# Performance work log

Hardware: AMD Instinct MI355X
Metric: run time of the kernel (lower is better)

Reference implementation:

```python
import jax, jax.numpy as jnp
import numpy as np

N_TASKS = 32
SCALING = 32.0 / 16.0  # lora_alpha / r


def setup_inputs() -> dict:
    key = jax.random.key(0)
    k = jax.random.split(key, 6)
    B_, D_IN, D_OUT, R = 32768, 1024, 1024, 16
    x = jax.random.normal(k[0], (B_, D_IN), dtype=jnp.float32)
    task_ids = jax.random.randint(k[1], (B_,), 0, N_TASKS, dtype=jnp.int32)
    W_base = jax.random.normal(k[2], (D_OUT, D_IN), dtype=jnp.float32) * 0.02
    b_base = jax.random.normal(k[3], (D_OUT,), dtype=jnp.float32) * 0.02
    A = jax.random.normal(k[4], (N_TASKS, R, D_IN), dtype=jnp.float32) * 0.02
    B = jax.random.normal(k[5], (N_TASKS, D_OUT, R), dtype=jnp.float32) * 0.02
    return {"x": x, "task_ids": task_ids, "W_base": W_base, "b_base": b_base, "A": A, "B": B}


def reference(x, task_ids, W_base, b_base, A, B):
    # Base linear: [B, D_in] @ [D_in, D_out] + bias
    result = x @ W_base.T + b_base
    # Per-example task routing. Equivalent to gathering A[t], B[t] per row,
    # expressed as a masked dense contraction over the small task axis.
    onehot = jax.nn.one_hot(task_ids, N_TASKS, dtype=x.dtype)  # [B, T]
    # down-projection for every task, then mask to the selected task: [B, T, r]
    ax = jnp.einsum('bi,tri->btr', x, A) * onehot[:, :, None]
    # up-projection contracting out the task axis: [B, D_out]
    lora_out = jnp.einsum('btr,tor->bo', ax, B) * SCALING
    return result + lora_out
```

## Files before the change

kernel.cpp:

```cpp
#include <hip/hip_runtime.h>


#define D_IN   1024
#define D_OUTV 1024
#define NTASK  32
#define NROWS  32768
#define RLORA  16
#define SCALE  2.0f

typedef unsigned short u16;
typedef __attribute__((ext_vector_type(4))) unsigned short u16x4;
typedef __attribute__((ext_vector_type(8))) unsigned short u16x8;
typedef __attribute__((ext_vector_type(8))) short s16x8;
typedef __attribute__((ext_vector_type(4))) float f32x4;

#define WB_OFF   (0)
#define AB_OFF   (2*1024*1024)
#define BB_OFF   (3*1024*1024)
#define CNT_OFF  (4*1024*1024)
#define RIDX_OFF (CNT_OFF + 512)
#define XG_OFF   (8ull*1024*1024)

__device__ __forceinline__ u16 f2bf(float f) {
  union { float f; unsigned u; } v; v.f = f;
  unsigned r = v.u + 0x7fffu + ((v.u >> 16) & 1u);
  return (u16)(r >> 16);
}

__device__ __forceinline__ void gl2lds16(const void* g, void* s) {
  __builtin_amdgcn_global_load_lds(
      (const __attribute__((address_space(1))) unsigned*)g,
      (__attribute__((address_space(3))) unsigned*)s, 16, 0, 0);
}

__global__ void k_convert(const float* __restrict__ W, const float* __restrict__ A,
                          const float* __restrict__ B, u16* __restrict__ Wb,
                          u16* __restrict__ Ab, u16* __restrict__ Bb) {
  int g = blockIdx.x * blockDim.x + threadIdx.x;
  const int NW = D_OUTV * D_IN / 4;
  const int NA = NTASK * RLORA * D_IN / 4;
  const float* src; u16* dst; int idx;
  if (g < NW) { src = W; dst = Wb; idx = g; }
  else if (g < NW + NA) { src = A; dst = Ab; idx = g - NW; }
  else { src = B; dst = Bb; idx = g - NW - NA; }
  f32x4 v = *(const f32x4*)(src + (size_t)idx * 4);
  u16x4 o;
  o[0] = f2bf(v[0]); o[1] = f2bf(v[1]); o[2] = f2bf(v[2]); o[3] = f2bf(v[3]);
  *(u16x4*)(dst + (size_t)idx * 4) = o;
}

__global__ void k_hist(const int* __restrict__ tasks, int* __restrict__ cnt) {
  __shared__ int h[NTASK];
  int tid = threadIdx.x;
  if (tid < NTASK) h[tid] = 0;
  __syncthreads();
  atomicAdd(&h[tasks[blockIdx.x * 256 + tid]], 1);
  __syncthreads();
  if (tid < NTASK) atomicAdd(&cnt[tid], h[tid]);
}

__global__ void k_scan(int* __restrict__ cnt) {
  int t = threadIdx.x;
  int c = (t < NTASK) ? cnt[t] : 0;
  int v = c;
  for (int d = 1; d < NTASK; d <<= 1) {
    int u = __shfl_up(v, d, 64);
    if (t >= d) v += u;
  }
  if (t < NTASK) {
    int ex = v - c;
    cnt[64 + t] = ex;
    cnt[32 + t] = ex;
    if (t == NTASK - 1) cnt[64 + NTASK] = v;
  }
}

__global__ void k_scatter(const int* __restrict__ tasks, int* __restrict__ cnt,
                          int* __restrict__ ridx) {
  __shared__ int h[NTASK], basev[NTASK];
  int tid = threadIdx.x;
  int b = blockIdx.x * 256 + tid;
  int t = tasks[b];
  if (tid < NTASK) h[tid] = 0;
  __syncthreads();
  atomicAdd(&h[t], 1);
  __syncthreads();
  if (tid < NTASK) {
    basev[tid] = atomicAdd(&cnt[32 + tid], h[tid]);
    h[tid] = 0;
  }
  __syncthreads();
  int r = atomicAdd(&h[t], 1);
  ridx[basev[t] + r] = b;
}

__global__ void k_gatherx(const float* __restrict__ x, const int* __restrict__ ridx,
                          u16* __restrict__ xg) {
  int g = blockIdx.x * 256 + threadIdx.x;
  int pos = g >> 7;
  int c8  = (g & 127) << 3;
  int src = ridx[pos];
  f32x4 a = *(const f32x4*)(x + (size_t)src * D_IN + c8);
  f32x4 b = *(const f32x4*)(x + (size_t)src * D_IN + c8 + 4);
  u16x8 o;
  o[0] = f2bf(a[0]); o[1] = f2bf(a[1]); o[2] = f2bf(a[2]); o[3] = f2bf(a[3]);
  o[4] = f2bf(b[0]); o[5] = f2bf(b[1]); o[6] = f2bf(b[2]); o[7] = f2bf(b[3]);
  *(u16x8*)(xg + (size_t)pos * D_IN + c8) = o;
}

#define BM 256
#define BN 128
#define BK 64
#define NTHR 512
#define SLOTS 5
#define NWG (8 * NTASK * SLOTS)

#define XSZ (BM * BK)
#define WSZ (BN * BK)
#define ASZ (RLORA * BK)

__global__ __launch_bounds__(NTHR, 2) void k_main_c(
    const u16* __restrict__ xg, const float* __restrict__ bias,
    const u16* __restrict__ Wb, const u16* __restrict__ Ab, const u16* __restrict__ Bb,
    const int* __restrict__ cnt, const int* __restrict__ ridx,
    float* __restrict__ out) {
  __shared__ __align__(16) u16 smem[2 * XSZ + 2 * WSZ + 2 * ASZ];
  __shared__ u16 bls[BN * 32];
  __shared__ u16 axs[BM * 32];
  __shared__ int rowid_l[BM];
  u16* xs  = smem;
  u16* wls = smem + 2 * XSZ;
  u16* als = wls + 2 * WSZ;
  float* ostage = (float*)smem;

  const int tid = threadIdx.x;
  const int l   = tid & 63;
  const int w   = tid >> 6;
  const int wr  = w >> 1;
  const int wc  = w & 1;
  const int l15 = l & 15;
  const int lg  = l >> 4;

  const int flat = blockIdx.x;
  const int idx  = flat >> 3;
  const int task = (flat & 7) + ((idx & 3) << 3);
  const int rem  = idx >> 2;
  const int cb   = rem & 7;
  const int slot = rem >> 3;

  const int o0    = cnt[64 + task];
  const int count = cnt[64 + task + 1] - o0;
  const int base  = slot * BM;
  if (base >= count) return;

  auto stage = [&](int t, int bsel) {
    const int kk = t * BK;
    u16* xbuf = xs + bsel * XSZ;
    u16* wbuf = wls + bsel * WSZ;
    u16* abuf = als + bsel * ASZ;
#pragma unroll
    for (int i = 0; i < 4; i++) {
      int ch = i * NTHR + tid;
      int r = ch >> 3, c = ch & 7;
      int gr = o0 + base + r;
      if (gr > NROWS - 1) gr = NROWS - 1;
      gl2lds16(xg + (size_t)gr * D_IN + kk + ((c ^ (r & 7)) << 3), xbuf + ch * 8);
    }
#pragma unroll
    for (int i = 0; i < 2; i++) {
      int ch = i * NTHR + tid;
      int wrow = ch >> 3, c = ch & 7;
      gl2lds16(Wb + (size_t)(cb * BN + wrow) * D_IN + kk + ((c ^ (wrow & 7)) << 3),
               wbuf + ch * 8);
    }
    if (tid < 128) {
      int r = tid >> 3, c = tid & 7;
      gl2lds16(Ab + (size_t)(task * RLORA + r) * D_IN + kk + ((c ^ (r & 7)) << 3),
               abuf + tid * 8);
    }
  };

  f32x4 acc[4][4];
  f32x4 axc[4];
  const f32x4 z4 = {0.f, 0.f, 0.f, 0.f};
#pragma unroll
  for (int m = 0; m < 4; m++) {
    axc[m] = z4;
#pragma unroll
    for (int n = 0; n < 4; n++) acc[m][n] = z4;
  }

  stage(0, 0);
  for (int s = tid; s < BN * 4; s += NTHR) {
    int c = s >> 2, part = s & 3;
    u16x8 v = {0, 0, 0, 0, 0, 0, 0, 0};
    if (part < 2)
      v = *(const u16x8*)(Bb + ((size_t)(task * D_OUTV) + cb * BN + c) * RLORA + part * 8);
    *(u16x8*)&bls[c * 32 + ((part * 8) ^ ((c & 3) << 3))] = v;
  }
  for (int i = tid; i < BM * 32 / 8; i += NTHR) {
    u16x8 z = {0, 0, 0, 0, 0, 0, 0, 0};
    *(u16x8*)&axs[i * 8] = z;
  }
  if (tid < BM) {
    int s = base + tid;
    rowid_l[tid] = (s < count) ? ridx[o0 + s] : 0;
  }
  __syncthreads();

#pragma unroll 2
  for (int t = 0; t < D_IN / BK; ++t) {
    if (t < D_IN / BK - 1) stage(t + 1, (t + 1) & 1);
    const u16* xbuf = xs + (t & 1) * XSZ;
    const u16* wbuf = wls + (t & 1) * WSZ;
    const u16* abuf = als + (t & 1) * ASZ;
#pragma unroll
    for (int k0 = 0; k0 < BK; k0 += 32) {
      int kf = k0 + lg * 8;
      s16x8 xf[4], wf[4];
#pragma unroll
      for (int m = 0; m < 4; m++) {
        int row = wr * 64 + m * 16 + l15;
        xf[m] = *(const s16x8*)&xbuf[row * BK + (kf ^ ((row & 7) << 3))];
      }
#pragma unroll
      for (int n = 0; n < 4; n++) {
        int col = wc * 64 + n * 16 + l15;
        wf[n] = *(const s16x8*)&wbuf[col * BK + (kf ^ ((col & 7) << 3))];
      }
#pragma unroll
      for (int m = 0; m < 4; m++)
#pragma unroll
        for (int n = 0; n < 4; n++)
          acc[m][n] = __builtin_amdgcn_mfma_f32_16x16x32_bf16(xf[m], wf[n], acc[m][n], 0, 0, 0);
      if (wc == 0) {
        s16x8 af = *(const s16x8*)&abuf[l15 * BK + (kf ^ ((l15 & 7) << 3))];
#pragma unroll
        for (int m = 0; m < 4; m++)
          axc[m] = __builtin_amdgcn_mfma_f32_16x16x32_bf16(xf[m], af, axc[m], 0, 0, 0);
      }
    }
    __syncthreads();
  }

  if (wc == 0) {
#pragma unroll
    for (int m = 0; m < 4; m++) {
#pragma unroll
      for (int j = 0; j < 4; j++) {
        int row = wr * 64 + m * 16 + lg * 4 + j;
        axs[row * 32 + (l15 ^ ((row & 3) << 3))] = f2bf(axc[m][j] * SCALE);
      }
    }
  }
  __syncthreads();

  int kf2 = lg * 8;
  s16x8 axf[4], blf[4];
#pragma unroll
  for (int m = 0; m < 4; m++) {
    int row = wr * 64 + m * 16 + l15;
    axf[m] = *(const s16x8*)&axs[row * 32 + (kf2 ^ ((row & 3) << 3))];
  }
#pragma unroll
  for (int n = 0; n < 4; n++) {
    int col = wc * 64 + n * 16 + l15;
    blf[n] = *(const s16x8*)&bls[col * 32 + (kf2 ^ ((col & 3) << 3))];
  }
  float bv[4];
#pragma unroll
  for (int n = 0; n < 4; n++) bv[n] = bias[cb * BN + wc * 64 + n * 16 + l15];
#pragma unroll
  for (int n = 0; n < 4; n++)
#pragma unroll
    for (int m = 0; m < 4; m++) {
      acc[m][n] = __builtin_amdgcn_mfma_f32_16x16x32_bf16(axf[m], blf[n], acc[m][n], 0, 0, 0);
#pragma unroll
      for (int j = 0; j < 4; j++) acc[m][n][j] += bv[n];
    }

#pragma unroll
  for (int half = 0; half < 2; ++half) {
    __syncthreads();
    if ((wr >> 1) == half) {
#pragma unroll
      for (int m = 0; m < 4; m++)
#pragma unroll
        for (int n = 0; n < 4; n++)
#pragma unroll
          for (int j = 0; j < 4; j++) {
            int rl  = (wr & 1) * 64 + m * 16 + lg * 4 + j;
            int col = wc * 64 + n * 16 + l15;
            ostage[rl * 128 + (col ^ (((rl >> 2) & 3) << 3))] = acc[m][n][j];
          }
    }
    __syncthreads();
#pragma unroll
    for (int it = 0; it < 8; ++it) {
      int ch = it * NTHR + tid;
      int rl = ch >> 5;
      int cq = ch & 31;
      int lrow = half * 128 + rl;
      if (base + lrow < count) {
        int grow = rowid_l[lrow];
        f32x4 v = *(const f32x4*)&ostage[rl * 128 + ((cq * 4) ^ (((rl >> 2) & 3) << 3))];
        *(f32x4*)&out[(size_t)grow * D_OUTV + cb * BN + cq * 4] = v;
      }
    }
  }
}

extern "C" void kernel_launch(void* const* d_in, const int* in_sizes, int n_in,
                              void* d_out, int out_size, void* d_ws, size_t ws_size,
                              hipStream_t stream) {
  const float* x     = (const float*)d_in[0];
  const int*   tasks = (const int*)d_in[1];
  const float* W     = (const float*)d_in[2];
  const float* bias  = (const float*)d_in[3];
  const float* A     = (const float*)d_in[4];
  const float* B     = (const float*)d_in[5];
  float* out = (float*)d_out;
  char* ws = (char*)d_ws;
  u16* Wb = (u16*)(ws + WB_OFF);
  u16* Ab = (u16*)(ws + AB_OFF);
  u16* Bb = (u16*)(ws + BB_OFF);
  int* cnt  = (int*)(ws + CNT_OFF);
  int* ridx = (int*)(ws + RIDX_OFF);
  u16* xg   = (u16*)(ws + XG_OFF);

  hipMemsetAsync(cnt, 0, 512, stream);
  k_convert<<<2048, 256, 0, stream>>>(W, A, B, Wb, Ab, Bb);
  k_hist<<<NROWS / 256, 256, 0, stream>>>(tasks, cnt);
  k_scan<<<1, 64, 0, stream>>>(cnt);
  k_scatter<<<NROWS / 256, 256, 0, stream>>>(tasks, cnt, ridx);
  k_gatherx<<<NROWS * D_IN / 8 / 256, 256, 0, stream>>>(x, ridx, xg);
  k_main_c<<<NWG, NTHR, 0, stream>>>(xg, bias, Wb, Ab, Bb, cnt, ridx, out);
}
```

Baseline: 183.0 us.

## Preload LoRA A slice fully, use explicit vmcnt waits, write outputs directly

Loads the task's full 16x1024 LoRA A block into LDS once at the start instead of staging a 64-column slice per k-step. The per-iteration __syncthreads is replaced by raw s_barrier plus an explicit s_waitcnt vmcnt(6), which lets the next stage's global-to-LDS loads stay in flight while the current tile is computed. The LDS-staged coalesced float4 epilogue is dropped in favour of scattered scalar stores from MFMA registers. That removes two barriers and the staging traffic, but the stores become less coalesced and LDS use grows, which may hurt occupancy at two blocks per CU.

```diff
diff --git a/kernel.cpp b/kernel.cpp
--- a/kernel.cpp
+++ b/kernel.cpp
@@ -115,23 +115,22 @@
 #define SLOTS 5
 #define NWG (8 * NTASK * SLOTS)
 
-#define XSZ (BM * BK)
-#define WSZ (BN * BK)
-#define ASZ (RLORA * BK)
+#define XSZ  (BM * BK)
+#define WSZ  (BN * BK)
+#define ALSZ (RLORA * D_IN)
+#define NKS  (D_IN / BK)
 
 __global__ __launch_bounds__(NTHR, 2) void k_main_c(
     const u16* __restrict__ xg, const float* __restrict__ bias,
     const u16* __restrict__ Wb, const u16* __restrict__ Ab, const u16* __restrict__ Bb,
     const int* __restrict__ cnt, const int* __restrict__ ridx,
     float* __restrict__ out) {
-  __shared__ __align__(16) u16 smem[2 * XSZ + 2 * WSZ + 2 * ASZ];
+  __shared__ __align__(16) u16 xs[2 * XSZ];
+  __shared__ __align__(16) u16 wls[2 * WSZ];
+  __shared__ __align__(16) u16 als[ALSZ];
   __shared__ u16 bls[BN * 32];
   __shared__ u16 axs[BM * 32];
   __shared__ int rowid_l[BM];
-  u16* xs  = smem;
-  u16* wls = smem + 2 * XSZ;
-  u16* als = wls + 2 * WSZ;
-  float* ostage = (float*)smem;
 
   const int tid = threadIdx.x;
   const int l   = tid & 63;
@@ -157,7 +156,6 @@
     const int kk = t * BK;
     u16* xbuf = xs + bsel * XSZ;
     u16* wbuf = wls + bsel * WSZ;
-    u16* abuf = als + bsel * ASZ;
 #pragma unroll
     for (int i = 0; i < 4; i++) {
       int ch = i * NTHR + tid;
@@ -173,24 +171,8 @@
       gl2lds16(Wb + (size_t)(cb * BN + wrow) * D_IN + kk + ((c ^ (wrow & 7)) << 3),
                wbuf + ch * 8);
     }
-    if (tid < 128) {
-      int r = tid >> 3, c = tid & 7;
-      gl2lds16(Ab + (size_t)(task * RLORA + r) * D_IN + kk + ((c ^ (r & 7)) << 3),
-               abuf + tid * 8);
-    }
   };
 
-  f32x4 acc[4][4];
-  f32x4 axc[4];
-  const f32x4 z4 = {0.f, 0.f, 0.f, 0.f};
-#pragma unroll
-  for (int m = 0; m < 4; m++) {
-    axc[m] = z4;
-#pragma unroll
-    for (int n = 0; n < 4; n++) acc[m][n] = z4;
-  }
-
-  stage(0, 0);
   for (int s = tid; s < BN * 4; s += NTHR) {
     int c = s >> 2, part = s & 3;
     u16x8 v = {0, 0, 0, 0, 0, 0, 0, 0};
@@ -208,12 +190,41 @@
   }
   __syncthreads();
 
+#pragma unroll
+  for (int i = 0; i < 4; i++) {
+    int ch = i * NTHR + tid;
+    int r = ch >> 7, c = ch & 127;
+    gl2lds16(Ab + (size_t)(task * RLORA + r) * D_IN + ((c ^ (r & 7)) << 3),
+             als + ch * 8);
+  }
+  stage(0, 0);
+
+  f32x4 acc[4][4];
+  f32x4 axc[4];
+  const f32x4 z4 = {0.f, 0.f, 0.f, 0.f};
+#pragma unroll
+  for (int m = 0; m < 4; m++) {
+    axc[m] = z4;
+#pragma unroll
+    for (int n = 0; n < 4; n++) acc[m][n] = z4;
+  }
+
 #pragma unroll 2
-  for (int t = 0; t < D_IN / BK; ++t) {
-    if (t < D_IN / BK - 1) stage(t + 1, (t + 1) & 1);
+  for (int t = 0; t < NKS; ++t) {
+    asm volatile("" ::: "memory");
+    __builtin_amdgcn_s_barrier();
+    asm volatile("" ::: "memory");
+    if (t < NKS - 1) stage(t + 1, (t + 1) & 1);
+    if (t < NKS - 1) {
+      asm volatile("s_waitcnt vmcnt(6)" ::: "memory");
+    } else {
+      asm volatile("s_waitcnt vmcnt(0)" ::: "memory");
+    }
+    __builtin_amdgcn_s_barrier();
+    __builtin_amdgcn_sched_barrier(0);
+
     const u16* xbuf = xs + (t & 1) * XSZ;
     const u16* wbuf = wls + (t & 1) * WSZ;
-    const u16* abuf = als + (t & 1) * ASZ;
 #pragma unroll
     for (int k0 = 0; k0 < BK; k0 += 32) {
       int kf = k0 + lg * 8;
@@ -234,14 +245,15 @@
         for (int n = 0; n < 4; n++)
           acc[m][n] = __builtin_amdgcn_mfma_f32_16x16x32_bf16(xf[m], wf[n], acc[m][n], 0, 0, 0);
       if (wc == 0) {
-        s16x8 af = *(const s16x8*)&abuf[l15 * BK + (kf ^ ((l15 & 7) << 3))];
+        int kg = t * BK + kf;
+        s16x8 af = *(const s16x8*)&als[l15 * D_IN + (kg ^ ((l15 & 7) << 3))];
 #pragma unroll
         for (int m = 0; m < 4; m++)
           axc[m] = __builtin_amdgcn_mfma_f32_16x16x32_bf16(xf[m], af, axc[m], 0, 0, 0);
       }
     }
-    __syncthreads();
-  }
+  }
+  __syncthreads();
 
   if (wc == 0) {
 #pragma unroll
@@ -271,40 +283,18 @@
 #pragma unroll
   for (int n = 0; n < 4; n++) bv[n] = bias[cb * BN + wc * 64 + n * 16 + l15];
 #pragma unroll
-  for (int n = 0; n < 4; n++)
+  for (int n = 0; n < 4; n++) {
+    int colg = cb * BN + wc * 64 + n * 16 + l15;
 #pragma unroll
     for (int m = 0; m < 4; m++) {
-      acc[m][n] = __builtin_amdgcn_mfma_f32_16x16x32_bf16(axf[m], blf[n], acc[m][n], 0, 0, 0);
-#pragma unroll
-      for (int j = 0; j < 4; j++) acc[m][n][j] += bv[n];
-    }
-
-#pragma unroll
-  for (int half = 0; half < 2; ++half) {
-    __syncthreads();
-    if ((wr >> 1) == half) {
-#pragma unroll
-      for (int m = 0; m < 4; m++)
-#pragma unroll
-        for (int n = 0; n < 4; n++)
-#pragma unroll
-          for (int j = 0; j < 4; j++) {
-            int rl  = (wr & 1) * 64 + m * 16 + lg * 4 + j;
-            int col = wc * 64 + n * 16 + l15;
-            ostage[rl * 128 + (col ^ (((rl >> 2) & 3) << 3))] = acc[m][n][j];
-          }
-    }
-    __syncthreads();
-#pragma unroll
-    for (int it = 0; it < 8; ++it) {
-      int ch = it * NTHR + tid;
-      int rl = ch >> 5;
-      int cq = ch & 31;
-      int lrow = half * 128 + rl;
-      if (base + lrow < count) {
-        int grow = rowid_l[lrow];
-        f32x4 v = *(const f32x4*)&ostage[rl * 128 + ((cq * 4) ^ (((rl >> 2) & 3) << 3))];
-        *(f32x4*)&out[(size_t)grow * D_OUTV + cb * BN + cq * 4] = v;
+      f32x4 r = __builtin_amdgcn_mfma_f32_16x16x32_bf16(axf[m], blf[n], acc[m][n], 0, 0, 0);
+#pragma unroll
+      for (int j = 0; j < 4; j++) {
+        int lrow = wr * 64 + m * 16 + lg * 4 + j;
+        if (base + lrow < count) {
+          int grow = rowid_l[lrow];
+          out[(size_t)grow * D_OUTV + colg] = r[j] + bv[n];
+        }
       }
     }
   }
```

Result: slower. 199.1 us (+8.8%).
